# Kernel tuning notes

Hardware: AMD Instinct MI355X
Metric: run time of the kernel (lower is better)

The kernel has to match this reference:

```python
import jax, jax.numpy as jnp
import numpy as np

HIDDEN = 2048
N_HEADS = 32
N_KV_HEADS = 8
N_GROUPS = N_HEADS // N_KV_HEADS  # 4
HEAD_DIM = HIDDEN // N_HEADS      # 64
BATCH, SEQ = 2, 2048


def setup_inputs() -> dict:
    key = jax.random.key(0)
    ks = jax.random.split(key, 5)
    s = 0.02
    return {
        "x": jax.random.normal(ks[0], (BATCH, SEQ, HIDDEN), dtype=jnp.float32),
        "Wq": jax.random.normal(ks[1], (HIDDEN, HIDDEN), dtype=jnp.float32) * s,
        "Wk": jax.random.normal(ks[2], (N_KV_HEADS * HEAD_DIM, HIDDEN), dtype=jnp.float32) * s,
        "Wv": jax.random.normal(ks[3], (N_KV_HEADS * HEAD_DIM, HIDDEN), dtype=jnp.float32) * s,
        "Wo": jax.random.normal(ks[4], (HIDDEN, HIDDEN), dtype=jnp.float32) * s,
    }


def reference(x, Wq, Wk, Wv, Wo):
    b, s, _ = x.shape
    # Projections (nn.Linear: y = x @ W.T)
    q = (x @ Wq.T).reshape(b, s, N_KV_HEADS, N_GROUPS, HEAD_DIM)  # group heads by kv head
    k = (x @ Wk.T).reshape(b, s, N_KV_HEADS, HEAD_DIM)
    v = (x @ Wv.T).reshape(b, s, N_KV_HEADS, HEAD_DIM)
    scale = 1.0 / jnp.sqrt(jnp.asarray(HEAD_DIM, dtype=x.dtype))
    # Grouped scores: equivalent to repeat_interleave of K over groups
    scores = jnp.einsum('bqhgd,bkhd->bhgqk', q, k) * scale  # [b, kvh, g, s, s]
    causal_mask = jnp.triu(jnp.ones((s, s), dtype=bool), k=1)
    scores = jnp.where(causal_mask, -jnp.inf, scores)
    attn = jax.nn.softmax(scores, axis=-1)
    out = jnp.einsum('bhgqk,bkhd->bqhgd', attn, v)  # [b, s, kvh, g, hd]
    out = out.reshape(b, s, HIDDEN)
    return out @ Wo.T
```

## Files before the change

kernel.cpp:

```cpp
#include <hip/hip_runtime.h>

#define HIDDEN 2048
#define NHEADS 32
#define NKV 8
#define HD 64
#define BATCH 2
#define SEQ 2048
#define MROWS (BATCH*SEQ)
#define KVDIM (NKV*HD)
#define QKVN (HIDDEN + 2*KVDIM)

typedef __bf16 bf16x8 __attribute__((ext_vector_type(8)));
typedef float f32x4 __attribute__((ext_vector_type(4)));

__device__ inline void gld16(const __bf16* g, __bf16* l) {
    __builtin_amdgcn_global_load_lds((const __attribute__((address_space(1))) void*)g,
                                     (__attribute__((address_space(3))) void*)l, 16, 0, 0);
}

__global__ __launch_bounds__(256) void cast_all(const float* __restrict__ x,
                                                const float* __restrict__ wq,
                                                const float* __restrict__ wk,
                                                const float* __restrict__ wv,
                                                const float* __restrict__ wo,
                                                __bf16* __restrict__ xb,
                                                __bf16* __restrict__ wqkv,
                                                __bf16* __restrict__ wob,
                                                float qscale) {
    int blk = blockIdx.x;
    const float* src; __bf16* dst; float sc = 1.0f; size_t off;
    if (blk < 8192)        { src = x;  dst = xb;   off = (size_t)blk * 1024; }
    else if (blk < 12288)  { src = wq; dst = wqkv; off = (size_t)(blk - 8192) * 1024; sc = qscale; }
    else if (blk < 13312)  { src = wk; dst = wqkv + (size_t)HIDDEN * HIDDEN; off = (size_t)(blk - 12288) * 1024; }
    else if (blk < 14336)  { src = wv; dst = wqkv + (size_t)(HIDDEN + KVDIM) * HIDDEN; off = (size_t)(blk - 13312) * 1024; }
    else                   { src = wo; dst = wob;  off = (size_t)(blk - 14336) * 1024; }
    size_t i4 = off + (size_t)threadIdx.x * 4;
    float4 f = *(const float4*)(src + i4);
    dst[i4 + 0] = (__bf16)(f.x * sc);
    dst[i4 + 1] = (__bf16)(f.y * sc);
    dst[i4 + 2] = (__bf16)(f.z * sc);
    dst[i4 + 3] = (__bf16)(f.w * sc);
}

__device__ inline void store_val(__bf16* C, size_t idx, float v) { C[idx] = (__bf16)v; }
__device__ inline void store_val(float* C, size_t idx, float v) { C[idx] = v; }

template <typename OutT>
__global__ __launch_bounds__(256) void gemm128(const __bf16* __restrict__ A,
                                               const __bf16* __restrict__ B,
                                               OutT* __restrict__ C,
                                               int M, int N, int K) {
    __shared__ __bf16 As[2][128][32];
    __shared__ __bf16 Bs[2][128][32];
    const int tid  = threadIdx.x;
    const int lane = tid & 63;
    const int w    = tid >> 6;
    const int col  = lane & 15;
    const int quad = lane >> 4;
    const int m0 = blockIdx.y * 128;
    const int n0 = blockIdx.x * 128;
    const int wm = (w >> 1) * 64;
    const int wn = (w & 1) * 64;

    f32x4 acc[4][4];
    #pragma unroll
    for (int i = 0; i < 4; i++)
        #pragma unroll
        for (int j = 0; j < 4; j++) acc[i][j] = (f32x4){0.f,0.f,0.f,0.f};

    const int lrow = lane >> 2;
    const int lcol = (lane & 3) * 8;

    auto stage = [&](int k0, int buf) {
        #pragma unroll
        for (int c = 0; c < 4; c++) {
            int chunk = w * 4 + c;
            if (chunk < 8) {
                const __bf16* g = A + (size_t)(m0 + chunk*16 + lrow) * K + k0 + lcol;
                gld16(g, &As[buf][chunk*16][0]);
            } else {
                int bc = chunk - 8;
                const __bf16* g = B + (size_t)(n0 + bc*16 + lrow) * K + k0 + lcol;
                gld16(g, &Bs[buf][bc*16][0]);
            }
        }
    };

    const int nk = K / 32;
    stage(0, 0);
    for (int ki = 0; ki < nk; ki++) {
        const int buf = ki & 1;
        __syncthreads();
        if (ki + 1 < nk) stage((ki + 1) * 32, buf ^ 1);

        bf16x8 af[4], bfr[4];
        #pragma unroll
        for (int i = 0; i < 4; i++) af[i]  = *(const bf16x8*)&As[buf][wm + i*16 + col][quad*8];
        #pragma unroll
        for (int j = 0; j < 4; j++) bfr[j] = *(const bf16x8*)&Bs[buf][wn + j*16 + col][quad*8];
        #pragma unroll
        for (int i = 0; i < 4; i++)
            #pragma unroll
            for (int j = 0; j < 4; j++)
                acc[i][j] = __builtin_amdgcn_mfma_f32_16x16x32_bf16(af[i], bfr[j], acc[i][j], 0, 0, 0);
    }

    #pragma unroll
    for (int i = 0; i < 4; i++) {
        #pragma unroll
        for (int r = 0; r < 4; r++) {
            int mrow = m0 + wm + i*16 + quad*4 + r;
            size_t base = (size_t)mrow * N + n0 + wn;
            #pragma unroll
            for (int j = 0; j < 4; j++)
                store_val(C, base + j*16 + col, acc[i][j][r]);
        }
    }
}

__global__ __launch_bounds__(256) void transpose_v(const __bf16* __restrict__ QKV,
                                                   __bf16* __restrict__ VT) {
    __shared__ __bf16 tile[64][72];
    const int r0 = blockIdx.x * 64;
    const int s0 = blockIdx.y * 64;
    const int t  = threadIdx.x;
    #pragma unroll
    for (int cc = 0; cc < 2; cc++) {
        int c = t + cc * 256;
        int i = c >> 3;
        int j8 = (c & 7) * 8;
        bf16x8 v = *(const bf16x8*)(QKV + (size_t)(s0 + i) * QKVN + (HIDDEN + KVDIM) + r0 + j8);
        *(bf16x8*)&tile[i][j8] = v;
    }
    __syncthreads();
    #pragma unroll
    for (int cc = 0; cc < 2; cc++) {
        int c = t + cc * 256;
        int d = c >> 3;
        int sc = (c & 7) * 8;
        bf16x8 vv;
        #pragma unroll
        for (int j = 0; j < 8; j++) vv[j] = tile[sc + j][d];
        *(bf16x8*)(VT + (size_t)(r0 + d) * MROWS + s0 + sc) = vv;
    }
}

__global__ __launch_bounds__(256) void flash_attn(const __bf16* __restrict__ QKV,
                                                  const __bf16* __restrict__ VT,
                                                  __bf16* __restrict__ O) {
    const int p    = blockIdx.x & 15;
    const int head = (blockIdx.x >> 4) & 31;
    const int b    = blockIdx.x >> 9;
    const int kvh  = head >> 2;
    const int tid  = threadIdx.x;
    const int lane = tid & 63;
    const int w    = tid >> 6;
    const int col  = lane & 15;
    const int quad = lane >> 4;

    const int qbL = p * 64 + w * 16;
    const int qbH = (31 - p) * 64 + w * 16;
    const int np32 = (p + 1) * 2;
    const int nh32 = (32 - p) * 2;

    __shared__ __bf16 Ks[2][2][32][32];
    __shared__ __bf16 Vs[2][64][32];
    __shared__ __bf16 Pt[4][32][40];

    const size_t qL = (size_t)(b * SEQ + qbL + col) * QKVN + head * HD;
    const size_t qH = (size_t)(b * SEQ + qbH + col) * QKVN + head * HD;
    bf16x8 aqL0 = *(const bf16x8*)(QKV + qL + quad * 8);
    bf16x8 aqL1 = *(const bf16x8*)(QKV + qL + 32 + quad * 8);
    bf16x8 aqH0 = *(const bf16x8*)(QKV + qH + quad * 8);
    bf16x8 aqH1 = *(const bf16x8*)(QKV + qH + 32 + quad * 8);

    bf16x8 ones;
    #pragma unroll
    for (int j = 0; j < 8; j++) ones[j] = (__bf16)1.0f;

    f32x4 oL[4], oH[4];
    #pragma unroll
    for (int dn = 0; dn < 4; dn++) { oL[dn] = (f32x4){0.f,0.f,0.f,0.f}; oH[dn] = (f32x4){0.f,0.f,0.f,0.f}; }
    f32x4 lsumL = (f32x4){0.f,0.f,0.f,0.f};
    f32x4 lsumH = (f32x4){0.f,0.f,0.f,0.f};

    const int lrow = lane >> 2;
    const int lcol = (lane & 3) * 8;
    const size_t bS = (size_t)b * SEQ;

    auto stage = [&](int kbase, int buf) {
        #pragma unroll
        for (int c = 0; c < 2; c++) {
            int chunk = w * 2 + c;
            if (chunk < 4) {
                int h = chunk >> 1, half = chunk & 1;
                const __bf16* g = QKV + (bS + kbase + half*16 + lrow) * QKVN
                                      + HIDDEN + kvh * HD + h * 32 + lcol;
                gld16(g, &Ks[buf][h][half*16][0]);
            } else {
                int db = chunk - 4;
                const __bf16* g = VT + (size_t)(kvh * HD + db*16 + lrow) * MROWS
                                     + bS + kbase + lcol;
                gld16(g, &Vs[buf][db*16][0]);
            }
        }
    };

    stage(0, 0);
    for (int kt = 0; kt < nh32; kt++) {
        const int kbase = kt * 32;
        const int buf = kt & 1;
        const bool dual = (kt < np32);
        __syncthreads();
        if (kt + 1 < nh32) stage((kt + 1) * 32, buf ^ 1);

        f32x4 sH[2], sL[2];
        #pragma unroll
        for (int j = 0; j < 2; j++) { sH[j] = (f32x4){0.f,0.f,0.f,0.f}; sL[j] = (f32x4){0.f,0.f,0.f,0.f}; }
        #pragma unroll
        for (int j = 0; j < 2; j++) {
            bf16x8 bk0 = *(const bf16x8*)&Ks[buf][0][j*16 + col][quad*8];
            bf16x8 bk1 = *(const bf16x8*)&Ks[buf][1][j*16 + col][quad*8];
            sH[j] = __builtin_amdgcn_mfma_f32_16x16x32_bf16(aqH0, bk0, sH[j], 0, 0, 0);
            sH[j] = __builtin_amdgcn_mfma_f32_16x16x32_bf16(aqH1, bk1, sH[j], 0, 0, 0);
            if (dual) {
                sL[j] = __builtin_amdgcn_mfma_f32_16x16x32_bf16(aqL0, bk0, sL[j], 0, 0, 0);
                sL[j] = __builtin_amdgcn_mfma_f32_16x16x32_bf16(aqL1, bk1, sL[j], 0, 0, 0);
            }
        }

        if (kt >= nh32 - 2) {
            #pragma unroll
            for (int r = 0; r < 4; r++) {
                int qrow = qbH + quad*4 + r;
                #pragma unroll
                for (int j = 0; j < 2; j++)
                    if (kbase + j*16 + col > qrow) sH[j][r] = -1e30f;
            }
        }
        if (dual && kt >= np32 - 2) {
            #pragma unroll
            for (int r = 0; r < 4; r++) {
                int qrow = qbL + quad*4 + r;
                #pragma unroll
                for (int j = 0; j < 2; j++)
                    if (kbase + j*16 + col > qrow) sL[j][r] = -1e30f;
            }
        }

        #pragma unroll
        for (int r = 0; r < 4; r++) {
            int pr = quad*4 + r;
            #pragma unroll
            for (int j = 0; j < 2; j++)
                Pt[w][pr][j*16 + col] = (__bf16)__builtin_amdgcn_exp2f(sH[j][r]);
        }
        if (dual) {
            #pragma unroll
            for (int r = 0; r < 4; r++) {
                int pr = quad*4 + r;
                #pragma unroll
                for (int j = 0; j < 2; j++)
                    Pt[w][16 + pr][j*16 + col] = (__bf16)__builtin_amdgcn_exp2f(sL[j][r]);
            }
        }

        __asm__ volatile("s_waitcnt lgkmcnt(0)" ::: "memory");
        bf16x8 apH = *(const bf16x8*)&Pt[w][col][quad*8];
        lsumH = __builtin_amdgcn_mfma_f32_16x16x32_bf16(apH, ones, lsumH, 0, 0, 0);
        bf16x8 apL;
        if (dual) {
            apL = *(const bf16x8*)&Pt[w][16 + col][quad*8];
            lsumL = __builtin_amdgcn_mfma_f32_16x16x32_bf16(apL, ones, lsumL, 0, 0, 0);
        }

        #pragma unroll
        for (int dn = 0; dn < 4; dn++) {
            bf16x8 bv = *(const bf16x8*)&Vs[buf][dn*16 + col][quad*8];
            oH[dn] = __builtin_amdgcn_mfma_f32_16x16x32_bf16(apH, bv, oH[dn], 0, 0, 0);
            if (dual)
                oL[dn] = __builtin_amdgcn_mfma_f32_16x16x32_bf16(apL, bv, oL[dn], 0, 0, 0);
        }
    }

    #pragma unroll
    for (int r = 0; r < 4; r++) {
        float invL = 1.0f / lsumL[r];
        float invH = 1.0f / lsumH[r];
        __bf16* opL = O + (size_t)(b * SEQ + qbL + quad*4 + r) * HIDDEN + head * HD;
        __bf16* opH = O + (size_t)(b * SEQ + qbH + quad*4 + r) * HIDDEN + head * HD;
        #pragma unroll
        for (int dn = 0; dn < 4; dn++) {
            opL[dn*16 + col] = (__bf16)(oL[dn][r] * invL);
            opH[dn*16 + col] = (__bf16)(oH[dn][r] * invH);
        }
    }
}

extern "C" void kernel_launch(void* const* d_in, const int* in_sizes, int n_in,
                              void* d_out, int out_size, void* d_ws, size_t ws_size,
                              hipStream_t stream) {
    const float* x  = (const float*)d_in[0];
    const float* Wq = (const float*)d_in[1];
    const float* Wk = (const float*)d_in[2];
    const float* Wv = (const float*)d_in[3];
    const float* Wo = (const float*)d_in[4];
    float* out = (float*)d_out;

    __bf16* p    = (__bf16*)d_ws;
    __bf16* xb   = p; p += (size_t)MROWS * HIDDEN;
    __bf16* wqkv = p; p += (size_t)QKVN * HIDDEN;
    __bf16* wob  = p; p += (size_t)HIDDEN * HIDDEN;
    __bf16* qkv  = p; p += (size_t)MROWS * QKVN;
    __bf16* vt   = p; p += (size_t)KVDIM * MROWS;
    __bf16* aob  = xb;

    const float qscale = 0.125f * 1.4426950408889634f;
    cast_all<<<18432, 256, 0, stream>>>(x, Wq, Wk, Wv, Wo, xb, wqkv, wob, qscale);

    dim3 blk(256);
    gemm128<__bf16><<<dim3(QKVN/128, MROWS/128), blk, 0, stream>>>(xb, wqkv, qkv, MROWS, QKVN, HIDDEN);
    transpose_v<<<dim3(KVDIM/64, MROWS/64), blk, 0, stream>>>(qkv, vt);
    flash_attn<<<BATCH * NHEADS * (SEQ/128), blk, 0, stream>>>(qkv, vt, aob);
    gemm128<float><<<dim3(HIDDEN/128, MROWS/128), blk, 0, stream>>>(aob, wob, out, MROWS, HIDDEN, HIDDEN);
}
```

Measured before the change: 328.5 us.

## Triple-buffer K/V staging with swizzled LDS layout and MFMA priority hints

Moves the flash-attention K/V staging from double to triple buffering, with precomputed global pointers, so loads run two tiles ahead. The loop now waits on vmcnt and a raw s_barrier instead of __syncthreads. It XOR-swizzles the 16-byte column chunks in LDS to cut bank conflicts on the MFMA operand reads, and raises wave priority around the MFMA sections. The cost is more LDS per block, which may reduce occupancy, plus more delicate hand-written wait-count synchronisation.

New measurement: 330.4 us. No clear change (+0.6%).

```diff
diff --git a/kernel.cpp b/kernel.cpp
--- a/kernel.cpp
+++ b/kernel.cpp
@@ -163,8 +163,8 @@
     const int np32 = (p + 1) * 2;
     const int nh32 = (32 - p) * 2;
 
-    __shared__ __bf16 Ks[2][2][32][32];
-    __shared__ __bf16 Vs[2][64][32];
+    __shared__ __bf16 Ks[3][2][32][32];
+    __shared__ __bf16 Vs[3][64][32];
     __shared__ __bf16 Pt[4][32][40];
 
     const size_t qL = (size_t)(b * SEQ + qbL + col) * QKVN + head * HD;
@@ -185,42 +185,53 @@
     f32x4 lsumH = (f32x4){0.f,0.f,0.f,0.f};
 
     const int lrow = lane >> 2;
-    const int lcol = (lane & 3) * 8;
+    const int srcc8 = (((lane & 3) ^ (lrow & 3)) * 8);
+    const int swz   = (quad ^ (col & 3)) * 8;
     const size_t bS = (size_t)b * SEQ;
 
-    auto stage = [&](int kbase, int buf) {
-        #pragma unroll
-        for (int c = 0; c < 2; c++) {
-            int chunk = w * 2 + c;
-            if (chunk < 4) {
-                int h = chunk >> 1, half = chunk & 1;
-                const __bf16* g = QKV + (bS + kbase + half*16 + lrow) * QKVN
-                                      + HIDDEN + kvh * HD + h * 32 + lcol;
-                gld16(g, &Ks[buf][h][half*16][0]);
-            } else {
-                int db = chunk - 4;
-                const __bf16* g = VT + (size_t)(kvh * HD + db*16 + lrow) * MROWS
-                                     + bS + kbase + lcol;
-                gld16(g, &Vs[buf][db*16][0]);
-            }
-        }
+    const __bf16 *g0, *g1;
+    size_t gstep;
+    if (w < 2) {
+        g0 = QKV + (bS + lrow) * QKVN + HIDDEN + kvh * HD + w * 32 + srcc8;
+        g1 = g0 + (size_t)16 * QKVN;
+        gstep = (size_t)32 * QKVN;
+    } else {
+        g0 = VT + (size_t)(kvh * HD + (w - 2) * 32 + lrow) * MROWS + bS + srcc8;
+        g1 = g0 + (size_t)16 * MROWS;
+        gstep = 32;
+    }
+
+    auto stage = [&](int sb) {
+        if (w < 2) {
+            gld16(g0, &Ks[sb][w][0][0]);
+            gld16(g1, &Ks[sb][w][16][0]);
+        } else {
+            gld16(g0, &Vs[sb][(w - 2) * 32][0]);
+            gld16(g1, &Vs[sb][(w - 2) * 32 + 16][0]);
+        }
+        g0 += gstep; g1 += gstep;
     };
 
-    stage(0, 0);
+    stage(0);
+    stage(1);
+    int cur = 0, nx2 = 2;
     for (int kt = 0; kt < nh32; kt++) {
         const int kbase = kt * 32;
-        const int buf = kt & 1;
         const bool dual = (kt < np32);
-        __syncthreads();
-        if (kt + 1 < nh32) stage((kt + 1) * 32, buf ^ 1);
+        if (kt + 1 < nh32) { __asm__ volatile("s_waitcnt vmcnt(2)" ::: "memory"); }
+        else               { __asm__ volatile("s_waitcnt vmcnt(0)" ::: "memory"); }
+        __builtin_amdgcn_s_barrier();
+        __asm__ volatile("" ::: "memory");
+        if (kt + 2 < nh32) stage(nx2);
 
         f32x4 sH[2], sL[2];
         #pragma unroll
         for (int j = 0; j < 2; j++) { sH[j] = (f32x4){0.f,0.f,0.f,0.f}; sL[j] = (f32x4){0.f,0.f,0.f,0.f}; }
+        __builtin_amdgcn_s_setprio(1);
         #pragma unroll
         for (int j = 0; j < 2; j++) {
-            bf16x8 bk0 = *(const bf16x8*)&Ks[buf][0][j*16 + col][quad*8];
-            bf16x8 bk1 = *(const bf16x8*)&Ks[buf][1][j*16 + col][quad*8];
+            bf16x8 bk0 = *(const bf16x8*)&Ks[cur][0][j*16 + col][swz];
+            bf16x8 bk1 = *(const bf16x8*)&Ks[cur][1][j*16 + col][swz];
             sH[j] = __builtin_amdgcn_mfma_f32_16x16x32_bf16(aqH0, bk0, sH[j], 0, 0, 0);
             sH[j] = __builtin_amdgcn_mfma_f32_16x16x32_bf16(aqH1, bk1, sH[j], 0, 0, 0);
             if (dual) {
@@ -228,6 +239,7 @@
                 sL[j] = __builtin_amdgcn_mfma_f32_16x16x32_bf16(aqL1, bk1, sL[j], 0, 0, 0);
             }
         }
+        __builtin_amdgcn_s_setprio(0);
 
         if (kt >= nh32 - 2) {
             #pragma unroll
@@ -267,6 +279,7 @@
 
         __asm__ volatile("s_waitcnt lgkmcnt(0)" ::: "memory");
         bf16x8 apH = *(const bf16x8*)&Pt[w][col][quad*8];
+        __builtin_amdgcn_s_setprio(1);
         lsumH = __builtin_amdgcn_mfma_f32_16x16x32_bf16(apH, ones, lsumH, 0, 0, 0);
         bf16x8 apL;
         if (dual) {
@@ -276,11 +289,15 @@
 
         #pragma unroll
         for (int dn = 0; dn < 4; dn++) {
-            bf16x8 bv = *(const bf16x8*)&Vs[buf][dn*16 + col][quad*8];
+            bf16x8 bv = *(const bf16x8*)&Vs[cur][dn*16 + col][swz];
             oH[dn] = __builtin_amdgcn_mfma_f32_16x16x32_bf16(apH, bv, oH[dn], 0, 0, 0);
             if (dual)
                 oL[dn] = __builtin_amdgcn_mfma_f32_16x16x32_bf16(apL, bv, oL[dn], 0, 0, 0);
         }
+        __builtin_amdgcn_s_setprio(0);
+
+        cur = (cur == 2) ? 0 : cur + 1;
+        nx2 = (nx2 == 2) ? 0 : nx2 + 1;
     }
 
     #pragma unroll
```
